# Kernel tuning notes

Hardware: AMD Instinct MI355X
Metric: run time of the kernel (lower is better)

Reference implementation:

```python
import jax, jax.numpy as jnp
import numpy as np

D_MODEL = 1024
NUM_HEADS = 16
HEAD_DIM = D_MODEL // NUM_HEADS


def setup_inputs() -> dict:
    key = jax.random.key(0)
    ks = jax.random.split(key, 8)
    B, L, D = 4, 4096, D_MODEL
    s = 1.0 / np.sqrt(D)
    return {
        "x": jax.random.normal(ks[0], (B, L, D), dtype=jnp.float32),
        "y": jax.random.normal(ks[1], (B, L, D), dtype=jnp.float32),
        "Wkv": jax.random.normal(ks[2], (D, 2 * D), dtype=jnp.float32) * s,
        "bkv": jnp.zeros((2 * D,), dtype=jnp.float32),
        "Wq": jax.random.normal(ks[3], (D, D), dtype=jnp.float32) * s,
        "bq": jnp.zeros((D,), dtype=jnp.float32),
        "Wo": jax.random.normal(ks[4], (D, D), dtype=jnp.float32) * s,
        "bo": jnp.zeros((D,), dtype=jnp.float32),
    }


def reference(x, y, Wkv, bkv, Wq, bq, Wo, bo):
    B, L, D = x.shape
    H, hd = NUM_HEADS, HEAD_DIM
    # projections (torch Linear: x @ W^T + b; here W stored as [in,out])
    kv = (x @ Wkv + bkv).reshape(B, L, H, 2 * hd)
    q = (y @ Wq + bq).reshape(B, L, H, hd)
    # NOTE: source's permute() results are discarded, so attention is taken
    # over the HEADS axis at each position: attn shape [B, L, H, H].
    k, v = jnp.split(kv, 2, axis=-1)  # each [B, L, H, hd]
    scale = 1.0 / np.sqrt(hd)
    attn = jnp.einsum("blhd,blgd->blhg", q, k) * scale  # [B,L,H,H]
    attn = jax.nn.softmax(attn, axis=-1)
    val = jnp.einsum("blhg,blgd->blhd", attn, v).reshape(B, L, D)
    return val @ Wo + bo
```

## Files before the change

kernel.cpp:

```cpp
#include <hip/hip_runtime.h>
#include <math.h>


typedef __attribute__((ext_vector_type(8))) short bf16x8;
typedef __attribute__((ext_vector_type(4))) float f32x4;

__device__ __forceinline__ float b2f(short s) {
    union { unsigned u; float f; } x;
    x.u = ((unsigned)(unsigned short)s) << 16;
    return x.f;
}
__device__ __forceinline__ short f2b(float f) {
    union { float f; unsigned u; } x;
    x.f = f;
    unsigned r = (x.u + 0x7FFFu + ((x.u >> 16) & 1u)) >> 16;
    return (short)r;
}

__global__ __launch_bounds__(256) void cast2_f32_bf16(
    const float* __restrict__ in0, short* __restrict__ out0,
    const float* __restrict__ in1, short* __restrict__ out1, int n) {
    int i = (blockIdx.x * 256 + threadIdx.x) * 4;
    const float* in = in0;
    short* out = out0;
    if (i >= n) {
        i -= n;
        in = in1;
        out = out1;
    }
    float4 v = *(const float4*)(in + i);
    short4 o;
    o.x = f2b(v.x); o.y = f2b(v.y); o.z = f2b(v.z); o.w = f2b(v.w);
    *(short4*)(out + i) = o;
}

__global__ __launch_bounds__(256) void transpose_cast2(
    const float* __restrict__ W0, short* __restrict__ Wt0,
    const float* __restrict__ W1, short* __restrict__ Wt1, int K, int N) {
    const float* W = blockIdx.z ? W1 : W0;
    short* Wt = blockIdx.z ? Wt1 : Wt0;
    __shared__ float tile[32][33];
    int tx = threadIdx.x;
    int ty = threadIdx.y;
    int bx = blockIdx.x * 32;
    int by = blockIdx.y * 32;
#pragma unroll
    for (int j = 0; j < 32; j += 8)
        tile[ty + j][tx] = W[(size_t)(by + ty + j) * N + bx + tx];
    __syncthreads();
#pragma unroll
    for (int j = 0; j < 32; j += 8)
        Wt[(size_t)(bx + ty + j) * K + by + tx] = f2b(tile[tx][ty + j]);
}

#define BM 128
#define BN 128
#define BK 32

#define GLD_LDS(g, l) \
    __builtin_amdgcn_global_load_lds( \
        (const __attribute__((address_space(1))) void*)(g), \
        (__attribute__((address_space(3))) void*)(l), 16, 0, 0)

template <int OUT_BF16>
__global__ __launch_bounds__(256) void gemm_bt(
    const short* __restrict__ A,
    const short* __restrict__ Bt,
    const float* __restrict__ bias,
    void* __restrict__ Cout,
    int M, int N, int K) {
    __shared__ short lA[BM * BK];
    __shared__ short lB[BN * BK];

    const int tid = threadIdx.x;

    const int NX = gridDim.x;
    int bxi, byi;
    {
        int lin = blockIdx.y * NX + blockIdx.x;
        int xcd = lin & 7;
        int j = lin >> 3;
        bxi = j % NX;
        byi = (j / NX) * 8 + xcd;
    }
    const int bn = bxi * BN;
    const int bm = byi * BM;

    const int lane = tid & 63;
    const int wave = tid >> 6;
    const int wm = (wave & 1) * 64;
    const int wn = (wave >> 1) * 64;
    const int fr = lane & 15;
    const int kq = lane >> 4;

    f32x4 acc[4][4];
#pragma unroll
    for (int i = 0; i < 4; ++i)
#pragma unroll
        for (int j = 0; j < 4; ++j) acc[i][j] = (f32x4){0.f, 0.f, 0.f, 0.f};

    const int srow = tid >> 2;
    const int scol = (tid & 3) * 8;
    const short* agp = A + (size_t)(bm + srow) * K + scol;
    const short* bgp = Bt + (size_t)(bn + srow) * K + scol;
    const size_t rstep = (size_t)64 * K;

    for (int k0 = 0; k0 < K; k0 += BK) {
        __syncthreads();
        GLD_LDS(agp + k0, &lA[tid * 8]);
        GLD_LDS(agp + k0 + rstep, &lA[2048 + tid * 8]);
        GLD_LDS(bgp + k0, &lB[tid * 8]);
        GLD_LDS(bgp + k0 + rstep, &lB[2048 + tid * 8]);
        __syncthreads();

        bf16x8 af[4], bfg[4];
#pragma unroll
        for (int mi = 0; mi < 4; ++mi)
            af[mi] = *(const bf16x8*)&lA[(wm + mi * 16 + fr) * BK + kq * 8];
#pragma unroll
        for (int ni = 0; ni < 4; ++ni)
            bfg[ni] = *(const bf16x8*)&lB[(wn + ni * 16 + fr) * BK + kq * 8];
#pragma unroll
        for (int mi = 0; mi < 4; ++mi)
#pragma unroll
            for (int ni = 0; ni < 4; ++ni)
                acc[mi][ni] = __builtin_amdgcn_mfma_f32_16x16x32_bf16(
                    af[mi], bfg[ni], acc[mi][ni], 0, 0, 0);
    }

#pragma unroll
    for (int ni = 0; ni < 4; ++ni) {
        const int col = bn + wn + ni * 16 + fr;
        const float bv = bias[col];
#pragma unroll
        for (int mi = 0; mi < 4; ++mi) {
            const int row0 = bm + wm + mi * 16 + kq * 4;
#pragma unroll
            for (int r = 0; r < 4; ++r) {
                float v = acc[mi][ni][r] + bv;
                if (OUT_BF16)
                    ((short*)Cout)[(size_t)(row0 + r) * N + col] = f2b(v);
                else
                    ((float*)Cout)[(size_t)(row0 + r) * N + col] = v;
            }
        }
    }
}

__global__ __launch_bounds__(256) void attn_kernel(
    const short* __restrict__ Q, const short* __restrict__ KV,
    short* __restrict__ VAL) {
    const int wave = threadIdx.x >> 6;
    const int lane = threadIdx.x & 63;
    const size_t p = (size_t)blockIdx.x * 4 + wave;
    const int dq = lane & 3;

    const bf16x8* qp = (const bf16x8*)(Q + p * 1024 + (size_t)lane * 16);
    bf16x8 q0 = qp[0], q1 = qp[1];
    float q[16];
#pragma unroll
    for (int j = 0; j < 8; ++j) {
        q[j] = b2f(q0[j]);
        q[8 + j] = b2f(q1[j]);
    }

    const short* kvb = KV + p * 2048;

    float s[16];
#pragma unroll
    for (int g = 0; g < 16; ++g) {
        const bf16x8* kp = (const bf16x8*)(kvb + g * 128 + dq * 16);
        bf16x8 k0 = kp[0], k1 = kp[1];
        float d = 0.f;
#pragma unroll
        for (int j = 0; j < 8; ++j) {
            d += q[j] * b2f(k0[j]);
            d += q[8 + j] * b2f(k1[j]);
        }
        s[g] = d;
    }
    float mx = -1e30f;
#pragma unroll
    for (int g = 0; g < 16; ++g) {
        s[g] += __shfl_xor(s[g], 1, 64);
        s[g] += __shfl_xor(s[g], 2, 64);
        s[g] *= 0.125f;
        mx = fmaxf(mx, s[g]);
    }
    float ssum = 0.f;
#pragma unroll
    for (int g = 0; g < 16; ++g) {
        s[g] = __expf(s[g] - mx);
        ssum += s[g];
    }
    const float inv = 1.0f / ssum;

    float vo[16];
#pragma unroll
    for (int j = 0; j < 16; ++j) vo[j] = 0.f;
#pragma unroll
    for (int g = 0; g < 16; ++g) {
        const float w = s[g] * inv;
        const bf16x8* vp = (const bf16x8*)(kvb + g * 128 + 64 + dq * 16);
        bf16x8 v0 = vp[0], v1 = vp[1];
#pragma unroll
        for (int j = 0; j < 8; ++j) {
            vo[j] += w * b2f(v0[j]);
            vo[8 + j] += w * b2f(v1[j]);
        }
    }

    bf16x8 o0, o1;
#pragma unroll
    for (int j = 0; j < 8; ++j) {
        o0[j] = f2b(vo[j]);
        o1[j] = f2b(vo[8 + j]);
    }
    bf16x8* op = (bf16x8*)(VAL + p * 1024 + (size_t)lane * 16);
    op[0] = o0;
    op[1] = o1;
}

extern "C" void kernel_launch(void* const* d_in, const int* in_sizes, int n_in,
                              void* d_out, int out_size, void* d_ws,
                              size_t ws_size, hipStream_t stream) {
    const float* x = (const float*)d_in[0];
    const float* y = (const float*)d_in[1];
    const float* Wkv = (const float*)d_in[2];
    const float* bkv = (const float*)d_in[3];
    const float* Wq = (const float*)d_in[4];
    const float* bq = (const float*)d_in[5];
    const float* Wo = (const float*)d_in[6];
    const float* bo = (const float*)d_in[7];
    float* out = (float*)d_out;

    const int D = 1024;
    const int M = 16384;

    char* ws = (char*)d_ws;
    short* Xb = (short*)(ws);
    short* Yb = (short*)(ws + 33554432);
    short* Wkvt = (short*)(ws + 67108864);
    short* Wqt = (short*)(ws + 71303168);
    short* Wot = (short*)(ws + 73400320);
    short* KV = (short*)(ws + 75497472);
    short* Q = Xb;
    short* VAL = Yb;

    const int n = M * D;

    cast2_f32_bf16<<<2 * n / 1024, 256, 0, stream>>>(x, Xb, y, Yb, n);
    transpose_cast2<<<dim3(2 * D / 32, D / 32, 1), dim3(32, 8), 0, stream>>>(
        Wkv, Wkvt, (const float*)0, (short*)0, D, 2 * D);
    transpose_cast2<<<dim3(D / 32, D / 32, 2), dim3(32, 8), 0, stream>>>(
        Wq, Wqt, Wo, Wot, D, D);

    gemm_bt<1><<<dim3(2 * D / BN, M / BM), 256, 0, stream>>>(
        Xb, Wkvt, bkv, KV, M, 2 * D, D);
    gemm_bt<1><<<dim3(D / BN, M / BM), 256, 0, stream>>>(
        Yb, Wqt, bq, Q, M, D, D);
    attn_kernel<<<M / 4, 256, 0, stream>>>(Q, KV, VAL);
    gemm_bt<0><<<dim3(D / BN, M / BM), 256, 0, stream>>>(
        VAL, Wot, bo, out, M, D, D);
}
```

Before: 431.8 us.

## Rewrite GEMM as 256x256 double-buffered LDS pipeline with swizzle and 8 waves

Replaces the 128x128x32 single-buffer GEMM with a 256x256x64 tile run by 512 threads. Two LDS buffers let global-to-LDS loads for the next k-step overlap with MFMA clusters on the current one. The change also adds an XOR swizzle against LDS bank conflicts, a new XCD-aware block remap, and setprio around the MFMA groups. In exchange it uses 128KB of LDS, higher register pressure from the 8x4 accumulators, and fewer workgroups (256 for the 1024-wide GEMMs), which may underfill the GPU.

```diff
diff --git a/kernel.cpp b/kernel.cpp
--- a/kernel.cpp
+++ b/kernel.cpp
@@ -53,88 +53,146 @@
         Wt[(size_t)(bx + ty + j) * K + by + tx] = f2b(tile[tx][ty + j]);
 }
 
-#define BM 128
-#define BN 128
-#define BK 32
-
-#define GLD_LDS(g, l) \
-    __builtin_amdgcn_global_load_lds( \
-        (const __attribute__((address_space(1))) void*)(g), \
+#define BM 256
+#define BN 256
+#define BK 64
+
+#define SUBOFF(c, ab, ks) (((((c) * 2 + (ab)) * 2 + (ks))) * 8192)
+
+#define GLD16(g, l)                                           \
+    __builtin_amdgcn_global_load_lds(                         \
+        (const __attribute__((address_space(1))) void*)(g),   \
         (__attribute__((address_space(3))) void*)(l), 16, 0, 0)
 
+#define STAGE_A(c, ks, kk)                                                   \
+    do {                                                                     \
+        GLD16(agp + (kk) + (ks) * 32, lbase + SUBOFF(c, 0, ks) * 2 + dst);   \
+        GLD16(agp + (kk) + (ks) * 32 + qstep,                                \
+              lbase + SUBOFF(c, 0, ks) * 2 + 8192 + dst);                    \
+    } while (0)
+
+#define STAGE_B(c, ks, kk)                                                   \
+    do {                                                                     \
+        GLD16(bgp + (kk) + (ks) * 32, lbase + SUBOFF(c, 1, ks) * 2 + dst);   \
+        GLD16(bgp + (kk) + (ks) * 32 + qstep,                                \
+              lbase + SUBOFF(c, 1, ks) * 2 + 8192 + dst);                    \
+    } while (0)
+
+#define MFMA_CLUSTER(MH)                                                     \
+    do {                                                                     \
+        asm volatile("s_waitcnt lgkmcnt(0)" ::: "memory");                   \
+        __builtin_amdgcn_sched_barrier(0);                                   \
+        __builtin_amdgcn_s_setprio(1);                                       \
+        _Pragma("unroll") for (int i_ = 0; i_ < 4; ++i_)                     \
+            _Pragma("unroll") for (int j_ = 0; j_ < 4; ++j_)                 \
+                acc[(MH) + i_][j_] = __builtin_amdgcn_mfma_f32_16x16x32_bf16(\
+                    af[i_], bf[j_], acc[(MH) + i_][j_], 0, 0, 0);            \
+        __builtin_amdgcn_s_setprio(0);                                       \
+    } while (0)
+
 template <int OUT_BF16>
-__global__ __launch_bounds__(256) void gemm_bt(
+__global__ __launch_bounds__(512, 2) void gemm_bt(
     const short* __restrict__ A,
     const short* __restrict__ Bt,
     const float* __restrict__ bias,
     void* __restrict__ Cout,
     int M, int N, int K) {
-    __shared__ short lA[BM * BK];
-    __shared__ short lB[BN * BK];
+    __shared__ __align__(16) short lds[65536];
 
     const int tid = threadIdx.x;
 
     const int NX = gridDim.x;
-    int bxi, byi;
-    {
-        int lin = blockIdx.y * NX + blockIdx.x;
-        int xcd = lin & 7;
-        int j = lin >> 3;
-        bxi = j % NX;
-        byi = (j / NX) * 8 + xcd;
-    }
-    const int bn = bxi * BN;
-    const int bm = byi * BM;
+    const int nwg = NX * gridDim.y;
+    int lin = blockIdx.y * NX + blockIdx.x;
+    lin = (lin & 7) * (nwg >> 3) + (lin >> 3);
+    const int bn = (lin % NX) * BN;
+    const int bm = (lin / NX) * BM;
 
     const int lane = tid & 63;
     const int wave = tid >> 6;
-    const int wm = (wave & 1) * 64;
-    const int wn = (wave >> 1) * 64;
+    const int wr = wave >> 2;
+    const int wc = wave & 3;
     const int fr = lane & 15;
     const int kq = lane >> 4;
-
-    f32x4 acc[4][4];
-#pragma unroll
-    for (int i = 0; i < 4; ++i)
+    const int rsw = (kq ^ ((fr >> 1) & 3)) << 3;
+    const int aro = (wr * 128 + fr) * 32 + rsw;
+    const int bro = (wc * 64 + fr) * 32 + rsw;
+
+    const int srow = tid >> 2;
+    const int sslot = ((tid & 3) ^ ((tid >> 3) & 3)) * 8;
+    const short* agp = A + (size_t)(bm + srow) * K + sslot;
+    const short* bgp = Bt + (size_t)(bn + srow) * K + sslot;
+    const size_t qstep = (size_t)128 * K;
+    char* const lbase = (char*)lds;
+    const int dst = tid * 16;
+
+    f32x4 acc[8][4];
+#pragma unroll
+    for (int i = 0; i < 8; ++i)
 #pragma unroll
         for (int j = 0; j < 4; ++j) acc[i][j] = (f32x4){0.f, 0.f, 0.f, 0.f};
 
-    const int srow = tid >> 2;
-    const int scol = (tid & 3) * 8;
-    const short* agp = A + (size_t)(bm + srow) * K + scol;
-    const short* bgp = Bt + (size_t)(bn + srow) * K + scol;
-    const size_t rstep = (size_t)64 * K;
-
-    for (int k0 = 0; k0 < K; k0 += BK) {
-        __syncthreads();
-        GLD_LDS(agp + k0, &lA[tid * 8]);
-        GLD_LDS(agp + k0 + rstep, &lA[2048 + tid * 8]);
-        GLD_LDS(bgp + k0, &lB[tid * 8]);
-        GLD_LDS(bgp + k0 + rstep, &lB[2048 + tid * 8]);
-        __syncthreads();
-
-        bf16x8 af[4], bfg[4];
-#pragma unroll
-        for (int mi = 0; mi < 4; ++mi)
-            af[mi] = *(const bf16x8*)&lA[(wm + mi * 16 + fr) * BK + kq * 8];
-#pragma unroll
-        for (int ni = 0; ni < 4; ++ni)
-            bfg[ni] = *(const bf16x8*)&lB[(wn + ni * 16 + fr) * BK + kq * 8];
-#pragma unroll
-        for (int mi = 0; mi < 4; ++mi)
-#pragma unroll
-            for (int ni = 0; ni < 4; ++ni)
-                acc[mi][ni] = __builtin_amdgcn_mfma_f32_16x16x32_bf16(
-                    af[mi], bfg[ni], acc[mi][ni], 0, 0, 0);
+    STAGE_A(0, 0, 0);
+    STAGE_B(0, 0, 0);
+    STAGE_A(0, 1, 0);
+    STAGE_B(0, 1, 0);
+    asm volatile("s_waitcnt vmcnt(4)" ::: "memory");
+    __builtin_amdgcn_s_barrier();
+
+    const int NT = K >> 6;
+    for (int t = 0; t < NT; ++t) {
+        const int c = t & 1, cn = c ^ 1;
+        const int knext = (t + 1 < NT ? t + 1 : t) << 6;
+        bf16x8 af[4], bf[4];
+        const short* la0 = &lds[SUBOFF(c, 0, 0) + aro];
+        const short* lb0 = &lds[SUBOFF(c, 1, 0) + bro];
+#pragma unroll
+        for (int i = 0; i < 4; ++i) af[i] = *(const bf16x8*)(la0 + i * 512);
+#pragma unroll
+        for (int j = 0; j < 4; ++j) bf[j] = *(const bf16x8*)(lb0 + j * 512);
+        STAGE_A(cn, 0, knext);
+        __builtin_amdgcn_sched_barrier(0);
+        __builtin_amdgcn_s_barrier();
+        MFMA_CLUSTER(0);
+        __builtin_amdgcn_s_barrier();
+#pragma unroll
+        for (int i = 0; i < 4; ++i)
+            af[i] = *(const bf16x8*)(la0 + (4 + i) * 512);
+        STAGE_B(cn, 0, knext);
+        __builtin_amdgcn_sched_barrier(0);
+        __builtin_amdgcn_s_barrier();
+        MFMA_CLUSTER(4);
+        asm volatile("s_waitcnt vmcnt(4)" ::: "memory");
+        __builtin_amdgcn_s_barrier();
+        const short* la1 = &lds[SUBOFF(c, 0, 1) + aro];
+        const short* lb1 = &lds[SUBOFF(c, 1, 1) + bro];
+#pragma unroll
+        for (int i = 0; i < 4; ++i) af[i] = *(const bf16x8*)(la1 + i * 512);
+#pragma unroll
+        for (int j = 0; j < 4; ++j) bf[j] = *(const bf16x8*)(lb1 + j * 512);
+        STAGE_A(cn, 1, knext);
+        __builtin_amdgcn_sched_barrier(0);
+        __builtin_amdgcn_s_barrier();
+        MFMA_CLUSTER(0);
+        __builtin_amdgcn_s_barrier();
+#pragma unroll
+        for (int i = 0; i < 4; ++i)
+            af[i] = *(const bf16x8*)(la1 + (4 + i) * 512);
+        STAGE_B(cn, 1, knext);
+        __builtin_amdgcn_sched_barrier(0);
+        __builtin_amdgcn_s_barrier();
+        MFMA_CLUSTER(4);
+        asm volatile("s_waitcnt vmcnt(4)" ::: "memory");
+        __builtin_amdgcn_s_barrier();
     }
 
 #pragma unroll
     for (int ni = 0; ni < 4; ++ni) {
-        const int col = bn + wn + ni * 16 + fr;
+        const int col = bn + wc * 64 + ni * 16 + fr;
         const float bv = bias[col];
 #pragma unroll
-        for (int mi = 0; mi < 4; ++mi) {
-            const int row0 = bm + wm + mi * 16 + kq * 4;
+        for (int mi = 0; mi < 8; ++mi) {
+            const int row0 = bm + wr * 128 + mi * 16 + kq * 4;
 #pragma unroll
             for (int r = 0; r < 4; ++r) {
                 float v = acc[mi][ni][r] + bv;
@@ -145,6 +203,7 @@
             }
         }
     }
+    asm volatile("s_waitcnt vmcnt(0)" ::: "memory");
 }
 
 __global__ __launch_bounds__(256) void attn_kernel(
@@ -255,11 +314,11 @@
     transpose_cast2<<<dim3(D / 32, D / 32, 2), dim3(32, 8), 0, stream>>>(
         Wq, Wqt, Wo, Wot, D, D);
 
-    gemm_bt<1><<<dim3(2 * D / BN, M / BM), 256, 0, stream>>>(
+    gemm_bt<1><<<dim3(2 * D / BN, M / BM), 512, 0, stream>>>(
         Xb, Wkvt, bkv, KV, M, 2 * D, D);
-    gemm_bt<1><<<dim3(D / BN, M / BM), 256, 0, stream>>>(
+    gemm_bt<1><<<dim3(D / BN, M / BM), 512, 0, stream>>>(
         Yb, Wqt, bq, Q, M, D, D);
     attn_kernel<<<M / 4, 256, 0, stream>>>(Q, KV, VAL);
-    gemm_bt<0><<<dim3(D / BN, M / BM), 256, 0, stream>>>(
+    gemm_bt<0><<<dim3(D / BN, M / BM), 512, 0, stream>>>(
         VAL, Wot, bo, out, M, D, D);
 }
```

Result: faster. 395.3 us (-8.4%).
